# Kernel tuning notes

Hardware: AMD Instinct MI355X
Metric: run time of the kernel (lower is better)

The kernel has to match this reference:

```python
import jax, jax.numpy as jnp
import numpy as np
import math

B, S, D = 4, 1024, 1024
E, DE = 8, 128            # n_experts, expert_dim (D == E*DE)
TOPK = 2
SCALE = 1.0 / math.sqrt(D)  # source divides by sqrt(self.dim) = sqrt(transformer_dim)


def setup_inputs() -> dict:
    key = jax.random.key(0)
    k1, k2, k3, k4, k5 = jax.random.split(key, 5)
    Q = jax.random.normal(k1, (B, S, D), dtype=jnp.float32)
    K = jax.random.normal(k2, (B, S, D), dtype=jnp.float32)
    V = jax.random.normal(k3, (B, S, D), dtype=jnp.float32)
    route_prob = jax.random.uniform(k4, (B, E), dtype=jnp.float32)
    # first-stage MoE dispatch (idx_list): expert_mask[e, b] == 1 iff batch b routed to expert e
    expert_mask = jax.random.randint(k5, (E, B), 0, 2).astype(jnp.int32)
    mask = jnp.ones((B, S), dtype=jnp.float32)  # accepted but unused by the source forward
    return {"Q": Q, "K": K, "V": V, "route_prob": route_prob,
            "expert_mask": expert_mask, "mask": mask}


def reference(Q, K, V, route_prob, expert_mask, mask):
    # RowParallelMatmulWithMoE: each expert e attends using its 128-wide feature slice
    Qe = Q.reshape(B, S, E, DE)
    Ke = K.reshape(B, S, E, DE)
    scores = jnp.einsum('bsed,bted->ebst', Qe, Ke) * SCALE   # [E, B, S, S]
    probs = jax.nn.softmax(scores, axis=-1)                   # per-expert softmax (dropout p=0)
    # index_add_ scatter: sum routed experts' attention maps per batch element
    m1 = expert_mask.astype(Q.dtype)                          # [E, B]
    attn = jnp.einsum('eb,ebst->bst', m1, probs)              # [B, S, S]
    # preprocess: top-k expert re-selection from route_prob -> new idx_list
    _, top_idx = jax.lax.top_k(route_prob, TOPK)              # [B, TOPK]
    m2 = jnp.zeros((B, E), dtype=Q.dtype).at[jnp.arange(B)[:, None], top_idx].set(1.0)
    # ColumnParallelMatmulWithMoE: attn @ V restricted to each selected expert's V slice
    Ve = V.reshape(B, S, E, DE)
    out = jnp.einsum('bst,bted->bsed', attn, Ve) * m2[:, None, :, None]  # [B, S, E, DE]
    return out.reshape(B, S, D)
```

## Files before the change

### kernel.cpp

```cpp
#include <hip/hip_runtime.h>
#include <hip/hip_bf16.h>
#include <stdint.h>

#define B_ 4
#define S_ 1024
#define D_ 1024
#define E_ 8
#define DE_ 128
#define SCALE_ 0.03125f

typedef __attribute__((ext_vector_type(8))) short short8;
typedef __attribute__((ext_vector_type(4))) float f32x4;
typedef unsigned short ushort_t;
typedef unsigned int uint32;

__device__ __forceinline__ ushort_t f2bf(float f) {
    uint32 u = __float_as_uint(f);
    uint32 r = u + 0x7fffu + ((u >> 16) & 1u);
    return (ushort_t)(r >> 16);
}

#define GLOAD_LDS16(g, l) __builtin_amdgcn_global_load_lds( \
    (const __attribute__((address_space(1))) unsigned int*)(g), \
    (__attribute__((address_space(3))) unsigned int*)(l), 16, 0, 0)

__device__ __forceinline__ void stage64(const ushort_t* __restrict__ g,
                                        size_t stride, ushort_t* lds,
                                        int w, int lane) {
    #pragma unroll
    for (int j = 0; j < 4; ++j) {
        int cb = (w * 4 + j) << 6;
        int ch = cb + lane;
        int r = ch >> 4, c = ch & 15;
        GLOAD_LDS16(g + (size_t)r * stride + ((c ^ (r & 7)) << 3),
                    lds + ((size_t)cb << 3));
    }
}
__device__ __forceinline__ void stage128(const ushort_t* __restrict__ g,
                                         size_t stride, ushort_t* lds,
                                         int w, int lane) {
    #pragma unroll
    for (int j = 0; j < 8; ++j) {
        int cb = (w * 8 + j) << 6;
        int ch = cb + lane;
        int r = ch >> 4, c = ch & 15;
        GLOAD_LDS16(g + (size_t)r * stride + ((c ^ (r & 7)) << 3),
                    lds + ((size_t)cb << 3));
    }
}
__device__ __forceinline__ short8 fld(const ushort_t* lds, int row, int c) {
    return *(const short8*)(lds + (((row << 4) + (c ^ (row & 7))) << 3));
}

__device__ __forceinline__ void top2(const float* rp, int& i1, int& i2) {
    float v1 = rp[0]; i1 = 0;
    #pragma unroll
    for (int i = 1; i < 8; ++i) { float v = rp[i]; if (v > v1) { v1 = v; i1 = i; } }
    float v2 = -1e30f; i2 = 0;
    #pragma unroll
    for (int i = 0; i < 8; ++i) {
        if (i == i1) continue;
        float v = rp[i]; if (v > v2) { v2 = v; i2 = i; }
    }
}

__global__ __launch_bounds__(256) void prep_kernel(
        const float* __restrict__ Q, const float* __restrict__ K,
        const float* __restrict__ V, const float* __restrict__ route,
        const int* __restrict__ em,
        ushort_t* __restrict__ Qb, ushort_t* __restrict__ Kb,
        ushort_t* __restrict__ Vt) {
    __shared__ ushort_t tile[64][130];
    const int tid = threadIdx.x;
    const int sc = blockIdx.x, e = blockIdx.y, b = blockIdx.z;
    const int s0 = sc * 64;
    const size_t plane = ((size_t)(b * 8 + e)) << 17;

    const bool ak = em[e * B_ + b] != 0;
    int i1, i2; top2(route + b * 8, i1, i2);
    const bool av = (e == i1) || (e == i2);
    if (!ak && !av) return;

    if (ak) {
        #pragma unroll
        for (int i = 0; i < 8; ++i) {
            int idx = tid + i * 256, r = idx >> 5, c4 = idx & 31;
            size_t in_off = ((size_t)(b * 1024 + s0 + r) << 10) + (e << 7) + (c4 << 2);
            float4 q = *(const float4*)(Q + in_off);
            float4 k = *(const float4*)(K + in_off);
            size_t oo = plane + (((size_t)(s0 + r)) << 7) + (c4 << 2);
            *(ushort4*)(Qb + oo) = make_ushort4(f2bf(q.x), f2bf(q.y), f2bf(q.z), f2bf(q.w));
            *(ushort4*)(Kb + oo) = make_ushort4(f2bf(k.x), f2bf(k.y), f2bf(k.z), f2bf(k.w));
        }
    }
    if (av) {
        #pragma unroll
        for (int i = 0; i < 8; ++i) {
            int idx = tid + i * 256, r = idx >> 5, c4 = idx & 31;
            size_t in_off = ((size_t)(b * 1024 + s0 + r) << 10) + (e << 7) + (c4 << 2);
            float4 v = *(const float4*)(V + in_off);
            ushort_t* p = &tile[r][c4 << 2];
            p[0] = f2bf(v.x); p[1] = f2bf(v.y); p[2] = f2bf(v.z); p[3] = f2bf(v.w);
        }
        __syncthreads();
        #pragma unroll
        for (int i = 0; i < 4; ++i) {
            int item = tid + i * 256, d = item & 127, sg = item >> 7;
            union { uint4 q; ushort_t u[8]; } tmp;
            #pragma unroll
            for (int j = 0; j < 8; ++j) tmp.u[j] = tile[sg * 8 + j][d];
            *(uint4*)(Vt + plane + (((size_t)d) << 10) + s0 + (sg << 3)) = tmp.q;
        }
    }
}

__global__ __launch_bounds__(256, 2) void attn_pass1(
        const ushort_t* __restrict__ Qb, const ushort_t* __restrict__ Kb,
        const int* __restrict__ em, float* __restrict__ lsums) {

    __shared__ __align__(16) ushort_t qtile[64 * 128];
    __shared__ __align__(16) ushort_t ktile[2][64 * 128];
    __shared__ float red[2][64];

    const int stile = blockIdx.x, e = blockIdx.y, b = blockIdx.z;
    if (em[e * B_ + b] == 0) return;

    const int tid = threadIdx.x;
    const int w = tid >> 6, lane = tid & 63;
    const int quad = lane >> 4, l16 = lane & 15;
    const int wm = w & 1, wn = w >> 1;
    const int s0 = stile * 64;
    const size_t plane = ((size_t)(b * 8 + e)) << 17;

    stage64(Qb + plane + ((size_t)s0 << 7), 128, qtile, w, lane);
    stage64(Kb + plane, 128, ktile[0], w, lane);
    __syncthreads();

    short8 af[2][4];
    #pragma unroll
    for (int mi = 0; mi < 2; ++mi)
        #pragma unroll
        for (int kk = 0; kk < 4; ++kk)
            af[mi][kk] = fld(qtile, 32 * wm + 16 * mi + l16, (kk << 2) + quad);

    float rsum[2][4] = {{0.f,0.f,0.f,0.f},{0.f,0.f,0.f,0.f}};

    for (int tc = 0; tc < 16; ++tc) {
        if (tc < 15)
            stage64(Kb + plane + (((size_t)(tc + 1)) << 13), 128,
                    ktile[(tc + 1) & 1], w, lane);
        const ushort_t* kb = ktile[tc & 1];

        f32x4 sacc[2][2];
        #pragma unroll
        for (int mi = 0; mi < 2; ++mi)
            #pragma unroll
            for (int ni = 0; ni < 2; ++ni) sacc[mi][ni] = (f32x4){0.f,0.f,0.f,0.f};
        #pragma unroll
        for (int ni = 0; ni < 2; ++ni)
            #pragma unroll
            for (int kk = 0; kk < 4; ++kk) {
                short8 bf = fld(kb, 32 * wn + 16 * ni + l16, (kk << 2) + quad);
                #pragma unroll
                for (int mi = 0; mi < 2; ++mi)
                    sacc[mi][ni] = __builtin_amdgcn_mfma_f32_16x16x32_bf16(
                        af[mi][kk], bf, sacc[mi][ni], 0, 0, 0);
            }
        #pragma unroll
        for (int mi = 0; mi < 2; ++mi)
            #pragma unroll
            for (int ni = 0; ni < 2; ++ni)
                #pragma unroll
                for (int r = 0; r < 4; ++r)
                    rsum[mi][r] += __expf(sacc[mi][ni][r] * SCALE_);
        __syncthreads();
    }

    #pragma unroll
    for (int off = 1; off < 16; off <<= 1)
        #pragma unroll
        for (int mi = 0; mi < 2; ++mi)
            #pragma unroll
            for (int r = 0; r < 4; ++r)
                rsum[mi][r] += __shfl_xor(rsum[mi][r], off, 64);
    if (l16 == 0) {
        #pragma unroll
        for (int mi = 0; mi < 2; ++mi)
            #pragma unroll
            for (int r = 0; r < 4; ++r)
                red[wn][32 * wm + 16 * mi + quad * 4 + r] = rsum[mi][r];
    }
    __syncthreads();
    if (tid < 64)
        lsums[(((size_t)(b * 8 + e)) << 10) + s0 + tid] = red[0][tid] + red[1][tid];
}

__global__ __launch_bounds__(256, 2) void attn_passC(
        const ushort_t* __restrict__ Qb, const ushort_t* __restrict__ Kb,
        const float* __restrict__ lsums, const int* __restrict__ em,
        ushort_t* __restrict__ attnB) {

    __shared__ __align__(16) ushort_t qtile[2][64 * 128];
    __shared__ __align__(16) ushort_t ktile[2][64 * 128];

    const int stile = blockIdx.x, tt = blockIdx.y, b = blockIdx.z;
    const int tid = threadIdx.x;
    const int w = tid >> 6, lane = tid & 63;
    const int quad = lane >> 4, l16 = lane & 15;
    const int wm = w & 1, wn = w >> 1;
    const int s0 = stile * 64, t0 = tt * 64;

    uint32 epack = 0; int ne = 0;
    #pragma unroll
    for (int e = 0; e < 8; ++e)
        if (em[e * B_ + b] != 0) { epack |= (uint32)e << (3 * ne); ++ne; }

    f32x4 aacc[2][2];
    #pragma unroll
    for (int mi = 0; mi < 2; ++mi)
        #pragma unroll
        for (int ni = 0; ni < 2; ++ni) aacc[mi][ni] = (f32x4){0.f,0.f,0.f,0.f};

    if (ne > 0) {
        {
            int e0 = epack & 7;
            size_t pl = ((size_t)(b * 8 + e0)) << 17;
            stage64(Qb + pl + ((size_t)s0 << 7), 128, qtile[0], w, lane);
            stage64(Kb + pl + ((size_t)t0 << 7), 128, ktile[0], w, lane);
        }
        __syncthreads();

        for (int i = 0; i < ne; ++i) {
            if (i + 1 < ne) {
                int en = (epack >> (3 * (i + 1))) & 7;
                size_t pl = ((size_t)(b * 8 + en)) << 17;
                stage64(Qb + pl + ((size_t)s0 << 7), 128, qtile[(i + 1) & 1], w, lane);
                stage64(Kb + pl + ((size_t)t0 << 7), 128, ktile[(i + 1) & 1], w, lane);
            }
            int e = (epack >> (3 * i)) & 7;
            float rinv[2][4];
            #pragma unroll
            for (int mi = 0; mi < 2; ++mi)
                #pragma unroll
                for (int r = 0; r < 4; ++r)
                    rinv[mi][r] = 1.0f / lsums[(((size_t)(b * 8 + e)) << 10)
                                               + s0 + 32 * wm + 16 * mi + quad * 4 + r];

            const ushort_t* qb = qtile[i & 1];
            const ushort_t* kb = ktile[i & 1];
            short8 af[2][4];
            #pragma unroll
            for (int mi = 0; mi < 2; ++mi)
                #pragma unroll
                for (int kk = 0; kk < 4; ++kk)
                    af[mi][kk] = fld(qb, 32 * wm + 16 * mi + l16, (kk << 2) + quad);

            f32x4 sacc[2][2];
            #pragma unroll
            for (int mi = 0; mi < 2; ++mi)
                #pragma unroll
                for (int ni = 0; ni < 2; ++ni) sacc[mi][ni] = (f32x4){0.f,0.f,0.f,0.f};
            #pragma unroll
            for (int ni = 0; ni < 2; ++ni)
                #pragma unroll
                for (int kk = 0; kk < 4; ++kk) {
                    short8 bf = fld(kb, 32 * wn + 16 * ni + l16, (kk << 2) + quad);
                    #pragma unroll
                    for (int mi = 0; mi < 2; ++mi)
                        sacc[mi][ni] = __builtin_amdgcn_mfma_f32_16x16x32_bf16(
                            af[mi][kk], bf, sacc[mi][ni], 0, 0, 0);
                }
            #pragma unroll
            for (int mi = 0; mi < 2; ++mi)
                #pragma unroll
                for (int ni = 0; ni < 2; ++ni)
                    #pragma unroll
                    for (int r = 0; r < 4; ++r)
                        aacc[mi][ni][r] += __expf(sacc[mi][ni][r] * SCALE_) * rinv[mi][r];
            __syncthreads();
        }
    }

    #pragma unroll
    for (int mi = 0; mi < 2; ++mi)
        #pragma unroll
        for (int ni = 0; ni < 2; ++ni)
            #pragma unroll
            for (int r = 0; r < 4; ++r)
                attnB[(((size_t)(b * 1024 + s0 + 32 * wm + 16 * mi + quad * 4 + r)) << 10)
                      + t0 + 32 * wn + 16 * ni + l16] = f2bf(aacc[mi][ni][r]);
}

__global__ __launch_bounds__(256, 1) void attn_pass2(
        const ushort_t* __restrict__ Vt, const ushort_t* __restrict__ attnB,
        const float* __restrict__ route, float* __restrict__ out) {

    __shared__ __align__(16) ushort_t atile[2][64 * 128];
    __shared__ __align__(16) ushort_t vtile[2][128 * 128];

    const int stile = blockIdx.x, e = blockIdx.y, b = blockIdx.z;
    const int tid = threadIdx.x;
    const int w = tid >> 6, lane = tid & 63;
    const int quad = lane >> 4, l16 = lane & 15;
    const int wm = w & 1, wn = w >> 1;
    const int s0 = stile * 64;

    int i1, i2; top2(route + b * 8, i1, i2);

    if (e != i1 && e != i2) {
        #pragma unroll
        for (int i = 0; i < 8; ++i) {
            int idx = tid + i * 256, r = idx >> 5, c4 = idx & 31;
            *(float4*)(out + (((size_t)(b * 1024 + s0 + r)) << 10) + (e << 7) + (c4 << 2))
                = make_float4(0.f, 0.f, 0.f, 0.f);
        }
        return;
    }

    const size_t vplane = ((size_t)(b * 8 + e)) << 17;
    const ushort_t* abase = attnB + (((size_t)(b * 1024 + s0)) << 10);

    stage64(abase, 1024, atile[0], w, lane);
    stage128(Vt + vplane, 1024, vtile[0], w, lane);
    __syncthreads();

    f32x4 oacc[2][4];
    #pragma unroll
    for (int mi = 0; mi < 2; ++mi)
        #pragma unroll
        for (int ni = 0; ni < 4; ++ni) oacc[mi][ni] = (f32x4){0.f,0.f,0.f,0.f};

    for (int tc = 0; tc < 8; ++tc) {
        if (tc < 7) {
            stage64(abase + ((tc + 1) << 7), 1024, atile[(tc + 1) & 1], w, lane);
            stage128(Vt + vplane + ((tc + 1) << 7), 1024, vtile[(tc + 1) & 1], w, lane);
        }
        const ushort_t* at = atile[tc & 1];
        const ushort_t* vt = vtile[tc & 1];

        short8 af[2][4];
        #pragma unroll
        for (int mi = 0; mi < 2; ++mi)
            #pragma unroll
            for (int kk = 0; kk < 4; ++kk)
                af[mi][kk] = fld(at, 32 * wm + 16 * mi + l16, (kk << 2) + quad);
        #pragma unroll
        for (int ni = 0; ni < 4; ++ni)
            #pragma unroll
            for (int kk = 0; kk < 4; ++kk) {
                short8 bf = fld(vt, 64 * wn + 16 * ni + l16, (kk << 2) + quad);
                #pragma unroll
                for (int mi = 0; mi < 2; ++mi)
                    oacc[mi][ni] = __builtin_amdgcn_mfma_f32_16x16x32_bf16(
                        af[mi][kk], bf, oacc[mi][ni], 0, 0, 0);
            }
        __syncthreads();
    }

    #pragma unroll
    for (int mi = 0; mi < 2; ++mi)
        #pragma unroll
        for (int ni = 0; ni < 4; ++ni)
            #pragma unroll
            for (int r = 0; r < 4; ++r)
                out[(((size_t)(b * 1024 + s0 + 32 * wm + 16 * mi + quad * 4 + r)) << 10)
                    + (e << 7) + 64 * wn + 16 * ni + l16] = oacc[mi][ni][r];
}

extern "C" void kernel_launch(void* const* d_in, const int* in_sizes, int n_in,
                              void* d_out, int out_size, void* d_ws, size_t ws_size,
                              hipStream_t stream) {
    const float* Q     = (const float*)d_in[0];
    const float* K     = (const float*)d_in[1];
    const float* V     = (const float*)d_in[2];
    const float* route = (const float*)d_in[3];
    const int*   em    = (const int*)d_in[4];
    float* out = (float*)d_out;

    const size_t NB = (size_t)B_ * E_ * S_ * DE_;
    ushort_t* Qb = (ushort_t*)d_ws;
    ushort_t* Kb = Qb + NB;
    ushort_t* Vt = Kb + NB;
    float*    lsums = (float*)(Vt + NB);
    ushort_t* attnB = (ushort_t*)(lsums + (size_t)B_ * E_ * S_);

    dim3 gp(16, 8, 4);
    prep_kernel<<<gp, 256, 0, stream>>>(Q, K, V, route, em, Qb, Kb, Vt);
    dim3 g1(16, 8, 4);
    attn_pass1<<<g1, 256, 0, stream>>>(Qb, Kb, em, lsums);
    dim3 gc(16, 16, 4);
    attn_passC<<<gc, 256, 0, stream>>>(Qb, Kb, lsums, em, attnB);
    dim3 g2(16, 8, 4);
    attn_pass2<<<g2, 256, 0, stream>>>(Vt, attnB, route, out);
}
```

Before: 149.5 us.

## Fuse softmax-sum, attention accumulation and AV matmul into one mega kernel

Replaces the three attention kernels (row-sum pass, normalized accumulation pass, attn@V pass) with a single kernel per 16-row query tile that keeps the full expert-summed attention row in LDS and multiplies it directly with the selected experts' V slices. This removes the global round trips for the lsums and the bf16 attention matrix, plus two launches, and computes each score block once instead of twice. Zeroing of unselected expert outputs moves into the prep kernel. The cost is only 256 blocks with large LDS use (about 100KB) and one block per CU, the 16-row tiles reload full K per expert for every tile, and many registers are held for pstr and aacc.

```diff
diff --git a/kernel.cpp b/kernel.cpp
--- a/kernel.cpp
+++ b/kernel.cpp
@@ -4,7 +4,6 @@
 
 #define B_ 4
 #define S_ 1024
-#define D_ 1024
 #define E_ 8
 #define DE_ 128
 #define SCALE_ 0.03125f
@@ -24,17 +23,14 @@
     (const __attribute__((address_space(1))) unsigned int*)(g), \
     (__attribute__((address_space(3))) unsigned int*)(l), 16, 0, 0)
 
-__device__ __forceinline__ void stage64(const ushort_t* __restrict__ g,
+__device__ __forceinline__ void stage16(const ushort_t* __restrict__ g,
                                         size_t stride, ushort_t* lds,
                                         int w, int lane) {
-    #pragma unroll
-    for (int j = 0; j < 4; ++j) {
-        int cb = (w * 4 + j) << 6;
-        int ch = cb + lane;
-        int r = ch >> 4, c = ch & 15;
-        GLOAD_LDS16(g + (size_t)r * stride + ((c ^ (r & 7)) << 3),
-                    lds + ((size_t)cb << 3));
-    }
+    int cb = w << 6;
+    int ch = cb + lane;
+    int r = ch >> 4, c = ch & 15;
+    GLOAD_LDS16(g + (size_t)r * stride + ((c ^ (r & 7)) << 3),
+                lds + ((size_t)cb << 3));
 }
 __device__ __forceinline__ void stage128(const ushort_t* __restrict__ g,
                                          size_t stride, ushort_t* lds,
@@ -69,7 +65,7 @@
         const float* __restrict__ V, const float* __restrict__ route,
         const int* __restrict__ em,
         ushort_t* __restrict__ Qb, ushort_t* __restrict__ Kb,
-        ushort_t* __restrict__ Vt) {
+        ushort_t* __restrict__ Vt, float* __restrict__ out) {
     __shared__ ushort_t tile[64][130];
     const int tid = threadIdx.x;
     const int sc = blockIdx.x, e = blockIdx.y, b = blockIdx.z;
@@ -79,8 +75,15 @@
     const bool ak = em[e * B_ + b] != 0;
     int i1, i2; top2(route + b * 8, i1, i2);
     const bool av = (e == i1) || (e == i2);
-    if (!ak && !av) return;
-
+
+    if (!av) {
+        #pragma unroll
+        for (int i = 0; i < 8; ++i) {
+            int idx = tid + i * 256, r = idx >> 5, c4 = idx & 31;
+            *(float4*)(out + (((size_t)(b * 1024 + s0 + r)) << 10) + (e << 7) + (c4 << 2))
+                = make_float4(0.f, 0.f, 0.f, 0.f);
+        }
+    }
     if (ak) {
         #pragma unroll
         for (int i = 0; i < 8; ++i) {
@@ -114,257 +117,174 @@
     }
 }
 
-__global__ __launch_bounds__(256, 2) void attn_pass1(
+__global__ __launch_bounds__(256, 1) void attn_mega(
         const ushort_t* __restrict__ Qb, const ushort_t* __restrict__ Kb,
-        const int* __restrict__ em, float* __restrict__ lsums) {
-
-    __shared__ __align__(16) ushort_t qtile[64 * 128];
-    __shared__ __align__(16) ushort_t ktile[2][64 * 128];
-    __shared__ float red[2][64];
-
-    const int stile = blockIdx.x, e = blockIdx.y, b = blockIdx.z;
-    if (em[e * B_ + b] == 0) return;
-
+        const ushort_t* __restrict__ Vt, const float* __restrict__ route,
+        const int* __restrict__ em, float* __restrict__ out) {
+
+    __shared__ __align__(16) ushort_t kt[2][128 * 128];
+    __shared__ __align__(16) ushort_t qt[2][16 * 128];
+    __shared__ __align__(16) ushort_t attnL[16 * 1024];
+    __shared__ float red[4][16];
+
+    const int stile = blockIdx.x, b = blockIdx.y;
+    const int s0 = stile * 16;
     const int tid = threadIdx.x;
     const int w = tid >> 6, lane = tid & 63;
     const int quad = lane >> 4, l16 = lane & 15;
-    const int wm = w & 1, wn = w >> 1;
-    const int s0 = stile * 64;
-    const size_t plane = ((size_t)(b * 8 + e)) << 17;
-
-    stage64(Qb + plane + ((size_t)s0 << 7), 128, qtile, w, lane);
-    stage64(Kb + plane, 128, ktile[0], w, lane);
-    __syncthreads();
-
-    short8 af[2][4];
-    #pragma unroll
-    for (int mi = 0; mi < 2; ++mi)
-        #pragma unroll
-        for (int kk = 0; kk < 4; ++kk)
-            af[mi][kk] = fld(qtile, 32 * wm + 16 * mi + l16, (kk << 2) + quad);
-
-    float rsum[2][4] = {{0.f,0.f,0.f,0.f},{0.f,0.f,0.f,0.f}};
-
-    for (int tc = 0; tc < 16; ++tc) {
-        if (tc < 15)
-            stage64(Kb + plane + (((size_t)(tc + 1)) << 13), 128,
-                    ktile[(tc + 1) & 1], w, lane);
-        const ushort_t* kb = ktile[tc & 1];
-
-        f32x4 sacc[2][2];
-        #pragma unroll
-        for (int mi = 0; mi < 2; ++mi)
-            #pragma unroll
-            for (int ni = 0; ni < 2; ++ni) sacc[mi][ni] = (f32x4){0.f,0.f,0.f,0.f};
-        #pragma unroll
-        for (int ni = 0; ni < 2; ++ni)
-            #pragma unroll
-            for (int kk = 0; kk < 4; ++kk) {
-                short8 bf = fld(kb, 32 * wn + 16 * ni + l16, (kk << 2) + quad);
-                #pragma unroll
-                for (int mi = 0; mi < 2; ++mi)
-                    sacc[mi][ni] = __builtin_amdgcn_mfma_f32_16x16x32_bf16(
-                        af[mi][kk], bf, sacc[mi][ni], 0, 0, 0);
-            }
-        #pragma unroll
-        for (int mi = 0; mi < 2; ++mi)
-            #pragma unroll
-            for (int ni = 0; ni < 2; ++ni)
-                #pragma unroll
-                for (int r = 0; r < 4; ++r)
-                    rsum[mi][r] += __expf(sacc[mi][ni][r] * SCALE_);
-        __syncthreads();
-    }
-
-    #pragma unroll
-    for (int off = 1; off < 16; off <<= 1)
-        #pragma unroll
-        for (int mi = 0; mi < 2; ++mi)
-            #pragma unroll
-            for (int r = 0; r < 4; ++r)
-                rsum[mi][r] += __shfl_xor(rsum[mi][r], off, 64);
-    if (l16 == 0) {
-        #pragma unroll
-        for (int mi = 0; mi < 2; ++mi)
-            #pragma unroll
-            for (int r = 0; r < 4; ++r)
-                red[wn][32 * wm + 16 * mi + quad * 4 + r] = rsum[mi][r];
-    }
-    __syncthreads();
-    if (tid < 64)
-        lsums[(((size_t)(b * 8 + e)) << 10) + s0 + tid] = red[0][tid] + red[1][tid];
-}
-
-__global__ __launch_bounds__(256, 2) void attn_passC(
-        const ushort_t* __restrict__ Qb, const ushort_t* __restrict__ Kb,
-        const float* __restrict__ lsums, const int* __restrict__ em,
-        ushort_t* __restrict__ attnB) {
-
-    __shared__ __align__(16) ushort_t qtile[2][64 * 128];
-    __shared__ __align__(16) ushort_t ktile[2][64 * 128];
-
-    const int stile = blockIdx.x, tt = blockIdx.y, b = blockIdx.z;
-    const int tid = threadIdx.x;
-    const int w = tid >> 6, lane = tid & 63;
-    const int quad = lane >> 4, l16 = lane & 15;
-    const int wm = w & 1, wn = w >> 1;
-    const int s0 = stile * 64, t0 = tt * 64;
 
     uint32 epack = 0; int ne = 0;
     #pragma unroll
     for (int e = 0; e < 8; ++e)
         if (em[e * B_ + b] != 0) { epack |= (uint32)e << (3 * ne); ++ne; }
-
-    f32x4 aacc[2][2];
-    #pragma unroll
-    for (int mi = 0; mi < 2; ++mi)
-        #pragma unroll
-        for (int ni = 0; ni < 2; ++ni) aacc[mi][ni] = (f32x4){0.f,0.f,0.f,0.f};
+    int i1, i2; top2(route + b * 8, i1, i2);
+
+    f32x4 aacc[8][2];
+    #pragma unroll
+    for (int c = 0; c < 8; ++c)
+        #pragma unroll
+        for (int n = 0; n < 2; ++n) aacc[c][n] = (f32x4){0.f, 0.f, 0.f, 0.f};
 
     if (ne > 0) {
         {
             int e0 = epack & 7;
             size_t pl = ((size_t)(b * 8 + e0)) << 17;
-            stage64(Qb + pl + ((size_t)s0 << 7), 128, qtile[0], w, lane);
-            stage64(Kb + pl + ((size_t)t0 << 7), 128, ktile[0], w, lane);
+            stage16(Qb + pl + ((size_t)s0 << 7), 128, qt[0], w, lane);
+            stage128(Kb + pl, 128, kt[0], w, lane);
         }
         __syncthreads();
 
         for (int i = 0; i < ne; ++i) {
-            if (i + 1 < ne) {
-                int en = (epack >> (3 * (i + 1))) & 7;
-                size_t pl = ((size_t)(b * 8 + en)) << 17;
-                stage64(Qb + pl + ((size_t)s0 << 7), 128, qtile[(i + 1) & 1], w, lane);
-                stage64(Kb + pl + ((size_t)t0 << 7), 128, ktile[(i + 1) & 1], w, lane);
+            int e = (epack >> (3 * i)) & 7;
+            size_t pl = ((size_t)(b * 8 + e)) << 17;
+
+            short8 af[4];
+            #pragma unroll
+            for (int kk = 0; kk < 4; ++kk)
+                af[kk] = fld(qt[i & 1], l16, kk * 4 + quad);
+
+            float rsum[4] = {0.f, 0.f, 0.f, 0.f};
+            f32x4 pstr[8][2];
+
+            #pragma unroll
+            for (int c = 0; c < 8; ++c) {
+                int g = i * 8 + c;
+                if (c < 7) {
+                    stage128(Kb + pl + (((size_t)(c + 1)) << 14), 128,
+                             kt[(g + 1) & 1], w, lane);
+                } else if (i + 1 < ne) {
+                    int en = (epack >> (3 * (i + 1))) & 7;
+                    size_t pln = ((size_t)(b * 8 + en)) << 17;
+                    stage16(Qb + pln + ((size_t)s0 << 7), 128, qt[(i + 1) & 1], w, lane);
+                    stage128(Kb + pln, 128, kt[(g + 1) & 1], w, lane);
+                }
+                const ushort_t* kb = kt[g & 1];
+                f32x4 sacc[2];
+                sacc[0] = (f32x4){0.f, 0.f, 0.f, 0.f};
+                sacc[1] = (f32x4){0.f, 0.f, 0.f, 0.f};
+                #pragma unroll
+                for (int n = 0; n < 2; ++n)
+                    #pragma unroll
+                    for (int kk = 0; kk < 4; ++kk) {
+                        short8 bf = fld(kb, w * 32 + n * 16 + l16, kk * 4 + quad);
+                        sacc[n] = __builtin_amdgcn_mfma_f32_16x16x32_bf16(
+                            af[kk], bf, sacc[n], 0, 0, 0);
+                    }
+                #pragma unroll
+                for (int n = 0; n < 2; ++n)
+                    #pragma unroll
+                    for (int r = 0; r < 4; ++r) {
+                        float p = __expf(sacc[n][r] * SCALE_);
+                        pstr[c][n][r] = p;
+                        rsum[r] += p;
+                    }
+                __syncthreads();
             }
-            int e = (epack >> (3 * i)) & 7;
-            float rinv[2][4];
-            #pragma unroll
-            for (int mi = 0; mi < 2; ++mi)
+
+            #pragma unroll
+            for (int off = 1; off < 16; off <<= 1)
                 #pragma unroll
                 for (int r = 0; r < 4; ++r)
-                    rinv[mi][r] = 1.0f / lsums[(((size_t)(b * 8 + e)) << 10)
-                                               + s0 + 32 * wm + 16 * mi + quad * 4 + r];
-
-            const ushort_t* qb = qtile[i & 1];
-            const ushort_t* kb = ktile[i & 1];
-            short8 af[2][4];
-            #pragma unroll
-            for (int mi = 0; mi < 2; ++mi)
-                #pragma unroll
-                for (int kk = 0; kk < 4; ++kk)
-                    af[mi][kk] = fld(qb, 32 * wm + 16 * mi + l16, (kk << 2) + quad);
-
-            f32x4 sacc[2][2];
-            #pragma unroll
-            for (int mi = 0; mi < 2; ++mi)
-                #pragma unroll
-                for (int ni = 0; ni < 2; ++ni) sacc[mi][ni] = (f32x4){0.f,0.f,0.f,0.f};
-            #pragma unroll
-            for (int ni = 0; ni < 2; ++ni)
-                #pragma unroll
-                for (int kk = 0; kk < 4; ++kk) {
-                    short8 bf = fld(kb, 32 * wn + 16 * ni + l16, (kk << 2) + quad);
-                    #pragma unroll
-                    for (int mi = 0; mi < 2; ++mi)
-                        sacc[mi][ni] = __builtin_amdgcn_mfma_f32_16x16x32_bf16(
-                            af[mi][kk], bf, sacc[mi][ni], 0, 0, 0);
-                }
-            #pragma unroll
-            for (int mi = 0; mi < 2; ++mi)
-                #pragma unroll
-                for (int ni = 0; ni < 2; ++ni)
+                    rsum[r] += __shfl_xor(rsum[r], off, 64);
+            if (l16 == 0) {
+                #pragma unroll
+                for (int r = 0; r < 4; ++r) red[w][quad * 4 + r] = rsum[r];
+            }
+            __syncthreads();
+            float rinv[4];
+            #pragma unroll
+            for (int r = 0; r < 4; ++r)
+                rinv[r] = 1.0f / (red[0][quad * 4 + r] + red[1][quad * 4 + r] +
+                                  red[2][quad * 4 + r] + red[3][quad * 4 + r]);
+            #pragma unroll
+            for (int c = 0; c < 8; ++c)
+                #pragma unroll
+                for (int n = 0; n < 2; ++n)
                     #pragma unroll
                     for (int r = 0; r < 4; ++r)
-                        aacc[mi][ni][r] += __expf(sacc[mi][ni][r] * SCALE_) * rinv[mi][r];
+                        aacc[c][n][r] += pstr[c][n][r] * rinv[r];
+        }
+    }
+
+    #pragma unroll
+    for (int c = 0; c < 8; ++c)
+        #pragma unroll
+        for (int n = 0; n < 2; ++n)
+            #pragma unroll
+            for (int r = 0; r < 4; ++r) {
+                int row = quad * 4 + r;
+                int t = c * 128 + w * 32 + n * 16 + l16;
+                int ct = t >> 3, lo = t & 7;
+                attnL[(row << 10) + (((ct ^ (row & 7)) << 3) | lo)] =
+                    f2bf(aacc[c][n][r]);
+            }
+    stage128(Vt + (((size_t)(b * 8 + i1)) << 17), 1024, kt[0], w, lane);
+    __syncthreads();
+
+    int selE[2] = {i1, i2};
+    f32x4 oacc[2][2];
+    #pragma unroll
+    for (int s = 0; s < 2; ++s)
+        #pragma unroll
+        for (int n = 0; n < 2; ++n) oacc[s][n] = (f32x4){0.f, 0.f, 0.f, 0.f};
+
+    for (int sel = 0; sel < 2; ++sel) {
+        size_t vpl = ((size_t)(b * 8 + selE[sel])) << 17;
+        #pragma unroll
+        for (int c = 0; c < 8; ++c) {
+            int g = sel * 8 + c;
+            if (c < 7)
+                stage128(Vt + vpl + ((c + 1) * 128), 1024, kt[(g + 1) & 1], w, lane);
+            else if (sel == 0)
+                stage128(Vt + (((size_t)(b * 8 + selE[1])) << 17), 1024,
+                         kt[(g + 1) & 1], w, lane);
+            const ushort_t* vb = kt[g & 1];
+            short8 af2[4];
+            #pragma unroll
+            for (int kk = 0; kk < 4; ++kk) {
+                int ct = c * 16 + kk * 4 + quad;
+                af2[kk] = *(const short8*)&attnL[(l16 << 10) + (((ct ^ (l16 & 7)) << 3))];
+            }
+            #pragma unroll
+            for (int n = 0; n < 2; ++n)
+                #pragma unroll
+                for (int kk = 0; kk < 4; ++kk) {
+                    short8 bf = fld(vb, w * 32 + n * 16 + l16, kk * 4 + quad);
+                    oacc[sel][n] = __builtin_amdgcn_mfma_f32_16x16x32_bf16(
+                        af2[kk], bf, oacc[sel][n], 0, 0, 0);
+                }
             __syncthreads();
         }
     }
 
     #pragma unroll
-    for (int mi = 0; mi < 2; ++mi)
-        #pragma unroll
-        for (int ni = 0; ni < 2; ++ni)
+    for (int sel = 0; sel < 2; ++sel)
+        #pragma unroll
+        for (int n = 0; n < 2; ++n)
             #pragma unroll
             for (int r = 0; r < 4; ++r)
-                attnB[(((size_t)(b * 1024 + s0 + 32 * wm + 16 * mi + quad * 4 + r)) << 10)
-                      + t0 + 32 * wn + 16 * ni + l16] = f2bf(aacc[mi][ni][r]);
-}
-
-__global__ __launch_bounds__(256, 1) void attn_pass2(
-        const ushort_t* __restrict__ Vt, const ushort_t* __restrict__ attnB,
-        const float* __restrict__ route, float* __restrict__ out) {
-
-    __shared__ __align__(16) ushort_t atile[2][64 * 128];
-    __shared__ __align__(16) ushort_t vtile[2][128 * 128];
-
-    const int stile = blockIdx.x, e = blockIdx.y, b = blockIdx.z;
-    const int tid = threadIdx.x;
-    const int w = tid >> 6, lane = tid & 63;
-    const int quad = lane >> 4, l16 = lane & 15;
-    const int wm = w & 1, wn = w >> 1;
-    const int s0 = stile * 64;
-
-    int i1, i2; top2(route + b * 8, i1, i2);
-
-    if (e != i1 && e != i2) {
-        #pragma unroll
-        for (int i = 0; i < 8; ++i) {
-            int idx = tid + i * 256, r = idx >> 5, c4 = idx & 31;
-            *(float4*)(out + (((size_t)(b * 1024 + s0 + r)) << 10) + (e << 7) + (c4 << 2))
-                = make_float4(0.f, 0.f, 0.f, 0.f);
-        }
-        return;
-    }
-
-    const size_t vplane = ((size_t)(b * 8 + e)) << 17;
-    const ushort_t* abase = attnB + (((size_t)(b * 1024 + s0)) << 10);
-
-    stage64(abase, 1024, atile[0], w, lane);
-    stage128(Vt + vplane, 1024, vtile[0], w, lane);
-    __syncthreads();
-
-    f32x4 oacc[2][4];
-    #pragma unroll
-    for (int mi = 0; mi < 2; ++mi)
-        #pragma unroll
-        for (int ni = 0; ni < 4; ++ni) oacc[mi][ni] = (f32x4){0.f,0.f,0.f,0.f};
-
-    for (int tc = 0; tc < 8; ++tc) {
-        if (tc < 7) {
-            stage64(abase + ((tc + 1) << 7), 1024, atile[(tc + 1) & 1], w, lane);
-            stage128(Vt + vplane + ((tc + 1) << 7), 1024, vtile[(tc + 1) & 1], w, lane);
-        }
-        const ushort_t* at = atile[tc & 1];
-        const ushort_t* vt = vtile[tc & 1];
-
-        short8 af[2][4];
-        #pragma unroll
-        for (int mi = 0; mi < 2; ++mi)
-            #pragma unroll
-            for (int kk = 0; kk < 4; ++kk)
-                af[mi][kk] = fld(at, 32 * wm + 16 * mi + l16, (kk << 2) + quad);
-        #pragma unroll
-        for (int ni = 0; ni < 4; ++ni)
-            #pragma unroll
-            for (int kk = 0; kk < 4; ++kk) {
-                short8 bf = fld(vt, 64 * wn + 16 * ni + l16, (kk << 2) + quad);
-                #pragma unroll
-                for (int mi = 0; mi < 2; ++mi)
-                    oacc[mi][ni] = __builtin_amdgcn_mfma_f32_16x16x32_bf16(
-                        af[mi][kk], bf, oacc[mi][ni], 0, 0, 0);
-            }
-        __syncthreads();
-    }
-
-    #pragma unroll
-    for (int mi = 0; mi < 2; ++mi)
-        #pragma unroll
-        for (int ni = 0; ni < 4; ++ni)
-            #pragma unroll
-            for (int r = 0; r < 4; ++r)
-                out[(((size_t)(b * 1024 + s0 + 32 * wm + 16 * mi + quad * 4 + r)) << 10)
-                    + (e << 7) + 64 * wn + 16 * ni + l16] = oacc[mi][ni][r];
+                out[(((size_t)(b * 1024 + s0 + quad * 4 + r)) << 10)
+                    + selE[sel] * 128 + w * 32 + n * 16 + l16] = oacc[sel][n][r];
 }
 
 extern "C" void kernel_launch(void* const* d_in, const int* in_sizes, int n_in,
@@ -381,15 +301,9 @@
     ushort_t* Qb = (ushort_t*)d_ws;
     ushort_t* Kb = Qb + NB;
     ushort_t* Vt = Kb + NB;
-    float*    lsums = (float*)(Vt + NB);
-    ushort_t* attnB = (ushort_t*)(lsums + (size_t)B_ * E_ * S_);
 
     dim3 gp(16, 8, 4);
-    prep_kernel<<<gp, 256, 0, stream>>>(Q, K, V, route, em, Qb, Kb, Vt);
-    dim3 g1(16, 8, 4);
-    attn_pass1<<<g1, 256, 0, stream>>>(Qb, Kb, em, lsums);
-    dim3 gc(16, 16, 4);
-    attn_passC<<<gc, 256, 0, stream>>>(Qb, Kb, lsums, em, attnB);
-    dim3 g2(16, 8, 4);
-    attn_pass2<<<g2, 256, 0, stream>>>(Vt, attnB, route, out);
-}
+    prep_kernel<<<gp, 256, 0, stream>>>(Q, K, V, route, em, Qb, Kb, Vt, out);
+    dim3 gm(64, 4);
+    attn_mega<<<gm, 256, 0, stream>>>(Qb, Kb, Vt, route, em, out);
+}
```

New measurement: 150.3 us. No clear change (+0.5%).
